# Performance work log

Hardware: AMD Instinct MI355X
Metric: run time of the kernel (lower is better)

The kernel has to match this reference:

```python
import jax, jax.numpy as jnp
import numpy as np

N = 10000      # nodes
E = 160000     # edges (avg degree 16)
D = 128        # channels
H = 4          # heads
C = 128        # per-head dim (PyG: out_channels per head = channels)
HC = H * C
EPS_SOFTMAX = 1e-16
EPS_NORM = 1e-5


def setup_inputs() -> dict:
    key = jax.random.key(0)
    ks = jax.random.split(key, 12)
    s = 1.0 / np.sqrt(D)
    sb = 1.0 / np.sqrt(3 * D)
    return {
        "x": jax.random.normal(ks[0], (N, D), jnp.float32),
        "edge_index": jax.random.randint(ks[1], (2, E), 0, N, dtype=jnp.int64),
        "Wq": jax.random.normal(ks[2], (D, HC), jnp.float32) * s,
        "bq": jnp.zeros((HC,), jnp.float32),
        "Wk": jax.random.normal(ks[3], (D, HC), jnp.float32) * s,
        "bk": jnp.zeros((HC,), jnp.float32),
        "Wv": jax.random.normal(ks[4], (D, HC), jnp.float32) * s,
        "bv": jnp.zeros((HC,), jnp.float32),
        "Wskip": jax.random.normal(ks[5], (D, D), jnp.float32) * s,
        "bskip": jnp.zeros((D,), jnp.float32),
        "Wbeta": jax.random.normal(ks[6], (3 * D,), jnp.float32) * sb,  # lin_beta, bias=False
        "gn_weight": jnp.ones((D,), jnp.float32),
        "gn_bias": jnp.zeros((D,), jnp.float32),
        "gn_mean_scale": jnp.ones((D,), jnp.float32),
    }


def reference(x, edge_index, Wq, bq, Wk, bk, Wv, bv, Wskip, bskip, Wbeta,
              gn_weight, gn_bias, gn_mean_scale):
    n = x.shape[0]
    src, dst = edge_index[0], edge_index[1]  # messages flow src(j) -> dst(i)

    # Projections [N,H,C]
    q = (x @ Wq + bq).reshape(n, H, C)
    k = (x @ Wk + bk).reshape(n, H, C)
    v = (x @ Wv + bv).reshape(n, H, C)

    # Per-edge attention logits [E,H]
    alpha = jnp.einsum('ehc,ehc->eh', q[dst], k[src]) / jnp.sqrt(jnp.float32(C))

    # Segment softmax over incoming edges of each dst node
    amax = jax.ops.segment_max(alpha, dst, num_segments=n)       # [N,H]
    amax = jnp.where(jnp.isfinite(amax), amax, 0.0)
    ex = jnp.exp(alpha - amax[dst])                              # [E,H]
    denom = jax.ops.segment_sum(ex, dst, num_segments=n)         # [N,H]
    attn = ex / (denom[dst] + EPS_SOFTMAX)                       # [E,H]

    # Weighted scatter-aggregate, then mean over heads (concat=False)
    msgs = attn[:, :, None] * v[src]                             # [E,H,C]
    out = jax.ops.segment_sum(msgs, dst, num_segments=n)         # [N,H,C]
    out = out.mean(axis=1)                                       # [N,D]

    # Beta-gated skip (PyG: beta = sigmoid(lin_beta([out, x_r, out - x_r])))
    skip = x @ Wskip + bskip
    beta = jax.nn.sigmoid(jnp.concatenate([out, skip, out - skip], axis=-1) @ Wbeta)
    beta = beta[:, None]
    out = beta * skip + (1.0 - beta) * out

    # GraphNorm (single graph): (x - mean_scale*mean) / sqrt(var + eps) * w + b
    mean = out.mean(axis=0)
    centered = out - gn_mean_scale * mean
    var = (centered * centered).mean(axis=0)
    out = gn_weight * centered / jnp.sqrt(var + EPS_NORM) + gn_bias

    # GELU (exact) + residual (shapes match); dropout is identity in eval
    out = jax.nn.gelu(out, approximate=False)
    return out + x
```

## Files before the change

### kernel.cpp

```cpp
#include <hip/hip_runtime.h>
#include <hip/hip_bf16.h>
#include <math.h>

#define D_DIM 128
#define HC_DIM 512
#define CAP 128
#define REP 4

typedef __attribute__((ext_vector_type(8))) short bf16x8;
typedef __attribute__((ext_vector_type(4))) float f32x4;
typedef __attribute__((ext_vector_type(2))) float f32x2;
typedef __attribute__((ext_vector_type(2))) _Float16 h16x2;

static __device__ __forceinline__ unsigned short f2bf(float f) {
  unsigned u = __float_as_uint(f);
  unsigned r = (u + 0x7fffu + ((u >> 16) & 1u)) >> 16;
  return (unsigned short)r;
}
static __device__ __forceinline__ float bflo(unsigned u) {
  return __uint_as_float(u << 16);
}
static __device__ __forceinline__ float bfhi(unsigned u) {
  return __uint_as_float(u & 0xffff0000u);
}

__global__ void prep_kernel(const float* __restrict__ x,
                            const float* __restrict__ Wq, const float* __restrict__ Wk,
                            const float* __restrict__ Wv, const float* __restrict__ Wskip,
                            const float* __restrict__ bq, const float* __restrict__ bk,
                            const float* __restrict__ bv, const float* __restrict__ bskip,
                            unsigned short* __restrict__ xb,
                            unsigned short* __restrict__ wcat,
                            float* __restrict__ bcat,
                            int* __restrict__ zbase, int zwords, int N) {
  int t = blockIdx.x * 256 + threadIdx.x;
  int X4 = N * 32;
  if (t < X4) {
    float4 f = *(const float4*)&x[t * 4];
    ushort4 o;
    o.x = f2bf(f.x); o.y = f2bf(f.y); o.z = f2bf(f.z); o.w = f2bf(f.w);
    *(ushort4*)&xb[t * 4] = o;
  } else if (t < X4 + 1664 * 128) {
    int widx = t - X4;
    if (widx < 3 * 65536) {
      int segi = widx >> 16;
      int r = widx & 65535;
      int kk = r >> 9;
      int m = r & 511;
      const float* W = (segi == 0) ? Wq : (segi == 1) ? Wk : Wv;
      wcat[(size_t)(segi * 512 + m) * 128 + kk] = f2bf(W[kk * 512 + m]);
    } else {
      int r = widx - 3 * 65536;
      int kk = r >> 7;
      int m = r & 127;
      wcat[(size_t)(1536 + m) * 128 + kk] = f2bf(Wskip[kk * 128 + m]);
    }
  } else if (t < X4 + 1664 * 128 + 1664) {
    int b = t - X4 - 1664 * 128;
    bcat[b] = (b < 512) ? bq[b] : (b < 1024) ? bk[b - 512]
            : (b < 1536) ? bv[b - 1024] : bskip[b - 1536];
  } else if (t < X4 + 1664 * 128 + 1664 + zwords) {
    zbase[t - X4 - 1664 * 128 - 1664] = 0;
  }
}

__global__ __launch_bounds__(256) void gemm_mfma_kernel(
    const unsigned short* __restrict__ Xb, const unsigned short* __restrict__ Wt,
    const float* __restrict__ bcat, unsigned short* __restrict__ qb,
    unsigned short* __restrict__ kf, unsigned char* __restrict__ v8,
    float* __restrict__ skip,
    const int* __restrict__ src, const int* __restrict__ dst,
    int* __restrict__ cnt, int* __restrict__ bsrc, int N, int E) {
  const int tid = threadIdx.x;
  {
    int nblk = gridDim.x * gridDim.y;
    int lb = blockIdx.y * gridDim.x + blockIdx.x;
    int per = (E + nblk - 1) / nblk;
    int e0 = lb * per;
    int e1 = min(e0 + per, E);
    for (int e = e0 + tid; e < e1; e += 256) {
      int d = dst[e];
      int p = atomicAdd(&cnt[d], 1);
      if (p < CAP) bsrc[d * CAP + p] = src[e];
    }
  }
  const int wave = tid >> 6, lane = tid & 63;
  const int l16 = lane & 15, quad = lane >> 4;
  const int row0 = (blockIdx.x * 4 + wave) * 64;
  const int col0 = blockIdx.y * 64;

  const unsigned short* xrow[4];
#pragma unroll
  for (int i = 0; i < 4; ++i) {
    int r = row0 + i * 16 + l16;
    if (r >= N) r = N - 1;
    xrow[i] = Xb + (size_t)r * 128;
  }
  const unsigned short* wrow[4];
  float bias[4];
#pragma unroll
  for (int j = 0; j < 4; ++j) {
    int c = col0 + j * 16 + l16;
    wrow[j] = Wt + (size_t)c * 128;
    bias[j] = bcat[c];
  }

  f32x4 acc[4][4] = {};
#pragma unroll
  for (int kk = 0; kk < 4; ++kk) {
    int k0 = kk * 32 + quad * 8;
    bf16x8 a[4], b[4];
#pragma unroll
    for (int i = 0; i < 4; ++i) a[i] = *(const bf16x8*)(xrow[i] + k0);
#pragma unroll
    for (int j = 0; j < 4; ++j) b[j] = *(const bf16x8*)(wrow[j] + k0);
#pragma unroll
    for (int i = 0; i < 4; ++i)
#pragma unroll
      for (int j = 0; j < 4; ++j)
        acc[i][j] = __builtin_amdgcn_mfma_f32_16x16x32_bf16(a[i], b[j], acc[i][j], 0, 0, 0);
  }

  const int kind = (col0 < 512) ? 0 : (col0 < 1024) ? 1 : (col0 < 1536) ? 2 : 3;
#pragma unroll
  for (int i = 0; i < 4; ++i) {
#pragma unroll
    for (int reg = 0; reg < 4; ++reg) {
      int r = row0 + i * 16 + quad * 4 + reg;
      if (r < N) {
#pragma unroll
        for (int j = 0; j < 4; ++j) {
          int cidx = col0 + j * 16 + l16;
          float val = acc[i][j][reg] + bias[j];
          if (kind == 0) {
            qb[(size_t)r * 512 + cidx] = f2bf(val);
          } else if (kind == 1) {
            _Float16 hv = (_Float16)val;
            kf[(size_t)r * 512 + cidx - 512] = *(unsigned short*)&hv;
          } else if (kind == 2) {
            int pk = __builtin_amdgcn_cvt_pk_fp8_f32(val, val, 0, false);
            v8[(size_t)r * 512 + cidx - 1024] = (unsigned char)pk;
          } else {
            skip[(size_t)r * 128 + cidx - 1536] = val;
          }
        }
      }
    }
  }
}

__global__ __launch_bounds__(256) void attn_combine_kernel(
    const unsigned short* __restrict__ qb, const unsigned short* __restrict__ kf,
    const unsigned char* __restrict__ v8, const int* __restrict__ cnt,
    const int* __restrict__ bsrc, const float* __restrict__ skip,
    const float* __restrict__ Wbeta, float* __restrict__ out2,
    float* __restrict__ colsum, float* __restrict__ colsq, int N) {
  __shared__ int eL[4][CAP];
  __shared__ float redS[4][128];
  __shared__ float redQ[4][128];
  int tid = threadIdx.x;
  int w = tid >> 6, lane = tid & 63;
  int node = blockIdx.x * 4 + w;
  bool nv = node < N;
  int nc = nv ? node : (N - 1);
  int g = lane >> 4, j = lane & 15;

  int count = nv ? min(cnt[nc], CAP) : 0;
  const int* bp = bsrc + (size_t)nc * CAP;
  for (int i = lane; i < count; i += 64) eL[w][i] = bp[i];

  const float qscale = 0.08838834764831845f * 1.4426950408889634f;
  float am0 = 0.f, am1 = 0.f, am2 = 0.f, am3 = 0.f;
  float am4 = 0.f, am5 = 0.f, am6 = 0.f, am7 = 0.f;

#pragma unroll 1
  for (int h = 0; h < 4; ++h) {
    int4 qi = *(const int4*)(qb + (size_t)nc * 512 + h * 128 + j * 8);
    h16x2 qh0, qh1, qh2, qh3;
    qh0[0] = (_Float16)(bflo(qi.x) * qscale); qh0[1] = (_Float16)(bfhi(qi.x) * qscale);
    qh1[0] = (_Float16)(bflo(qi.y) * qscale); qh1[1] = (_Float16)(bfhi(qi.y) * qscale);
    qh2[0] = (_Float16)(bflo(qi.z) * qscale); qh2[1] = (_Float16)(bfhi(qi.z) * qscale);
    qh3[0] = (_Float16)(bflo(qi.w) * qscale); qh3[1] = (_Float16)(bfhi(qi.w) * qscale);

    const unsigned short* kb = kf + h * 128 + j * 8;
    const unsigned char* vb = v8 + h * 128 + j * 8;
    float lsum = 0.f;
    float o0 = 0.f, o1 = 0.f, o2 = 0.f, o3 = 0.f;
    float o4 = 0.f, o5 = 0.f, o6 = 0.f, o7 = 0.f;

    if (count > 0) {
      int e = eL[w][(g < count) ? g : 0];
      uint4 kw = *(const uint4*)(kb + (size_t)e * 512);
      uint2 vw = *(const uint2*)(vb + (size_t)e * 512);
      for (int idx = 0; idx < count; idx += 4) {
        int rem = count - idx;
        int nrem = rem - 4;
        int en = (nrem > 0) ? eL[w][idx + 4 + ((g < nrem) ? g : 0)] : e;
        uint4 kwn = *(const uint4*)(kb + (size_t)en * 512);
        uint2 vwn = *(const uint2*)(vb + (size_t)en * 512);
        float p = __builtin_amdgcn_fdot2(qh0, *(h16x2*)&kw.x, 0.f, false);
        p = __builtin_amdgcn_fdot2(qh1, *(h16x2*)&kw.y, p, false);
        p = __builtin_amdgcn_fdot2(qh2, *(h16x2*)&kw.z, p, false);
        p = __builtin_amdgcn_fdot2(qh3, *(h16x2*)&kw.w, p, false);
        p += __shfl_xor(p, 1);
        p += __shfl_xor(p, 2);
        p += __shfl_xor(p, 4);
        p += __shfl_xor(p, 8);
        float a = (g < rem) ? p : -1e30f;
        float wgt = exp2f(a);
        f32x2 v01 = __builtin_amdgcn_cvt_pk_f32_fp8(vw.x, false);
        f32x2 v23 = __builtin_amdgcn_cvt_pk_f32_fp8(vw.x, true);
        f32x2 v45 = __builtin_amdgcn_cvt_pk_f32_fp8(vw.y, false);
        f32x2 v67 = __builtin_amdgcn_cvt_pk_f32_fp8(vw.y, true);
        lsum += wgt;
        o0 += wgt * v01.x; o1 += wgt * v01.y;
        o2 += wgt * v23.x; o3 += wgt * v23.y;
        o4 += wgt * v45.x; o5 += wgt * v45.y;
        o6 += wgt * v67.x; o7 += wgt * v67.y;
        kw = kwn; vw = vwn; e = en;
      }
    }
    o0 += __shfl_xor(o0, 16); o0 += __shfl_xor(o0, 32);
    o1 += __shfl_xor(o1, 16); o1 += __shfl_xor(o1, 32);
    o2 += __shfl_xor(o2, 16); o2 += __shfl_xor(o2, 32);
    o3 += __shfl_xor(o3, 16); o3 += __shfl_xor(o3, 32);
    o4 += __shfl_xor(o4, 16); o4 += __shfl_xor(o4, 32);
    o5 += __shfl_xor(o5, 16); o5 += __shfl_xor(o5, 32);
    o6 += __shfl_xor(o6, 16); o6 += __shfl_xor(o6, 32);
    o7 += __shfl_xor(o7, 16); o7 += __shfl_xor(o7, 32);
    lsum += __shfl_xor(lsum, 16); lsum += __shfl_xor(lsum, 32);
    float inv = 0.25f / (lsum + 1e-16f);
    am0 += o0 * inv; am1 += o1 * inv; am2 += o2 * inv; am3 += o3 * inv;
    am4 += o4 * inv; am5 += o5 * inv; am6 += o6 * inv; am7 += o7 * inv;
  }

  float4 sl = *(const float4*)&skip[(size_t)nc * 128 + j * 8];
  float4 sh = *(const float4*)&skip[(size_t)nc * 128 + j * 8 + 4];
  float4 wal = *(const float4*)&Wbeta[j * 8];
  float4 wah = *(const float4*)&Wbeta[j * 8 + 4];
  float4 wbl = *(const float4*)&Wbeta[128 + j * 8];
  float4 wbh = *(const float4*)&Wbeta[128 + j * 8 + 4];
  float4 wcl = *(const float4*)&Wbeta[256 + j * 8];
  float4 wch = *(const float4*)&Wbeta[256 + j * 8 + 4];
  float p = am0 * wal.x + sl.x * wbl.x + (am0 - sl.x) * wcl.x
          + am1 * wal.y + sl.y * wbl.y + (am1 - sl.y) * wcl.y
          + am2 * wal.z + sl.z * wbl.z + (am2 - sl.z) * wcl.z
          + am3 * wal.w + sl.w * wbl.w + (am3 - sl.w) * wcl.w
          + am4 * wah.x + sh.x * wbh.x + (am4 - sh.x) * wch.x
          + am5 * wah.y + sh.y * wbh.y + (am5 - sh.y) * wch.y
          + am6 * wah.z + sh.z * wbh.z + (am6 - sh.z) * wch.z
          + am7 * wah.w + sh.w * wbh.w + (am7 - sh.w) * wch.w;
  p += __shfl_xor(p, 1); p += __shfl_xor(p, 2);
  p += __shfl_xor(p, 4); p += __shfl_xor(p, 8);
  float beta = 1.f / (1.f + __expf(-p));
  float ob = 1.f - beta;
  float vm = nv ? 1.f : 0.f;
  float oc0 = (beta * sl.x + ob * am0) * vm;
  float oc1 = (beta * sl.y + ob * am1) * vm;
  float oc2 = (beta * sl.z + ob * am2) * vm;
  float oc3 = (beta * sl.w + ob * am3) * vm;
  float oc4 = (beta * sh.x + ob * am4) * vm;
  float oc5 = (beta * sh.y + ob * am5) * vm;
  float oc6 = (beta * sh.z + ob * am6) * vm;
  float oc7 = (beta * sh.w + ob * am7) * vm;

  if (g == 0) {
    float4 lo; lo.x = oc0; lo.y = oc1; lo.z = oc2; lo.w = oc3;
    float4 hi; hi.x = oc4; hi.y = oc5; hi.z = oc6; hi.w = oc7;
    if (nv) {
      *(float4*)&out2[(size_t)node * 128 + j * 8] = lo;
      *(float4*)&out2[(size_t)node * 128 + j * 8 + 4] = hi;
    }
    *(float4*)&redS[w][j * 8] = lo;
    *(float4*)&redS[w][j * 8 + 4] = hi;
    float4 ql; ql.x = oc0 * oc0; ql.y = oc1 * oc1; ql.z = oc2 * oc2; ql.w = oc3 * oc3;
    float4 qh; qh.x = oc4 * oc4; qh.y = oc5 * oc5; qh.z = oc6 * oc6; qh.w = oc7 * oc7;
    *(float4*)&redQ[w][j * 8] = ql;
    *(float4*)&redQ[w][j * 8 + 4] = qh;
  }
  __syncthreads();
  if (w == 0) {
    int c = lane * 2;
    float s0 = redS[0][c] + redS[1][c] + redS[2][c] + redS[3][c];
    float s1 = redS[0][c + 1] + redS[1][c + 1] + redS[2][c + 1] + redS[3][c + 1];
    float q0 = redQ[0][c] + redQ[1][c] + redQ[2][c] + redQ[3][c];
    float q1 = redQ[0][c + 1] + redQ[1][c + 1] + redQ[2][c + 1] + redQ[3][c + 1];
    int slot = (blockIdx.x & (REP - 1)) * 128;
    atomicAdd(&colsum[slot + c], s0);
    atomicAdd(&colsum[slot + c + 1], s1);
    atomicAdd(&colsq[slot + c], q0);
    atomicAdd(&colsq[slot + c + 1], q1);
  }
}

__global__ void final_kernel(const float* __restrict__ out2,
                             const float* __restrict__ colsum,
                             const float* __restrict__ colsq,
                             const float* __restrict__ gnw,
                             const float* __restrict__ gnb,
                             const float* __restrict__ gnms,
                             const float* __restrict__ x,
                             float* __restrict__ y, int total2, float invN) {
  int i = blockIdx.x * 256 + threadIdx.x;
  if (i < total2) {
    int c = (i & 63) * 2;
    float2 cs; cs.x = 0.f; cs.y = 0.f;
    float2 cq; cq.x = 0.f; cq.y = 0.f;
#pragma unroll
    for (int s = 0; s < REP; ++s) {
      float2 t = *(const float2*)&colsum[s * 128 + c];
      float2 u = *(const float2*)&colsq[s * 128 + c];
      cs.x += t.x; cs.y += t.y;
      cq.x += u.x; cq.y += u.y;
    }
    float2 gw = *(const float2*)&gnw[c];
    float2 gb = *(const float2*)&gnb[c];
    float2 gs = *(const float2*)&gnms[c];
    float mean0 = cs.x * invN, mean1 = cs.y * invN;
    float var0 = cq.x * invN - mean0 * mean0 * gs.x * (2.f - gs.x);
    float var1 = cq.y * invN - mean1 * mean1 * gs.y * (2.f - gs.y);
    float mul0 = gw.x / sqrtf(var0 + 1e-5f);
    float mul1 = gw.y / sqrtf(var1 + 1e-5f);
    float2 o = *(const float2*)&out2[i * 2];
    float2 xx = *(const float2*)&x[i * 2];
    float t0 = (o.x - gs.x * mean0) * mul0 + gb.x;
    float t1 = (o.y - gs.y * mean1) * mul1 + gb.y;
    float g0 = 0.5f * t0 * (1.f + erff(t0 * 0.70710678118654752f));
    float g1 = 0.5f * t1 * (1.f + erff(t1 * 0.70710678118654752f));
    float2 r; r.x = g0 + xx.x; r.y = g1 + xx.y;
    *(float2*)&y[i * 2] = r;
  }
}

extern "C" void kernel_launch(void* const* d_in, const int* in_sizes, int n_in,
                              void* d_out, int out_size, void* d_ws, size_t ws_size,
                              hipStream_t stream) {
  const float* x     = (const float*)d_in[0];
  const int*   ei    = (const int*)d_in[1];
  const float* Wq    = (const float*)d_in[2];
  const float* bq    = (const float*)d_in[3];
  const float* Wk    = (const float*)d_in[4];
  const float* bk    = (const float*)d_in[5];
  const float* Wv    = (const float*)d_in[6];
  const float* bv    = (const float*)d_in[7];
  const float* Wskip = (const float*)d_in[8];
  const float* bskip = (const float*)d_in[9];
  const float* Wbeta = (const float*)d_in[10];
  const float* gnw   = (const float*)d_in[11];
  const float* gnb   = (const float*)d_in[12];
  const float* gnms  = (const float*)d_in[13];

  const int N = in_sizes[0] / D_DIM;
  const int E = in_sizes[1] / 2;
  const int* src = ei;
  const int* dst = ei + E;

  char* p = (char*)d_ws;
  unsigned short* qb = (unsigned short*)p; p += (size_t)N * 512 * 2;
  unsigned short* kf = (unsigned short*)p; p += (size_t)N * 512 * 2;
  unsigned char*  v8 = (unsigned char*)p;  p += (size_t)N * 512;
  float*          skip = (float*)p;        p += (size_t)N * 128 * 4;
  float*          out2 = (float*)p;        p += (size_t)N * 128 * 4;
  int*   cnt    = (int*)p;   p += (size_t)N * 4;
  float* colsum = (float*)p; p += REP * 128 * 4;
  float* colsq  = (float*)p; p += REP * 128 * 4;
  int zwords = N + 2 * REP * 128;
  int* bsrc   = (int*)p;   p += (size_t)N * CAP * 4;
  unsigned short* wcat = (unsigned short*)p; p += (size_t)1664 * 128 * 2;
  float* bcat = (float*)p; p += 1664 * 4;
  unsigned short* xb = (unsigned short*)out2;

  int prepTotal = N * 32 + 1664 * 128 + 1664 + zwords;
  prep_kernel<<<(prepTotal + 255) / 256, 256, 0, stream>>>(
      x, Wq, Wk, Wv, Wskip, bq, bk, bv, bskip, xb, wcat, bcat, cnt, zwords, N);

  gemm_mfma_kernel<<<dim3(40, 26), 256, 0, stream>>>(
      xb, wcat, bcat, qb, kf, v8, skip, src, dst, cnt, bsrc, N, E);

  attn_combine_kernel<<<(N + 3) / 4, 256, 0, stream>>>(
      qb, kf, v8, cnt, bsrc, skip, Wbeta, out2, colsum, colsq, N);

  int total2 = N * D_DIM / 2;
  final_kernel<<<(total2 + 255) / 256, 256, 0, stream>>>(
      out2, colsum, colsq, gnw, gnb, gnms, x, (float*)d_out, total2, 1.f / (float)N);
}
```

Baseline: 183.6 us.

## Process all four heads in one edge loop instead of per-head passes

```diff
diff --git a/kernel.cpp b/kernel.cpp
--- a/kernel.cpp
+++ b/kernel.cpp
@@ -170,68 +170,93 @@
   for (int i = lane; i < count; i += 64) eL[w][i] = bp[i];
 
   const float qscale = 0.08838834764831845f * 1.4426950408889634f;
-  float am0 = 0.f, am1 = 0.f, am2 = 0.f, am3 = 0.f;
-  float am4 = 0.f, am5 = 0.f, am6 = 0.f, am7 = 0.f;
-
-#pragma unroll 1
+  h16x2 qh[4][4];
+#pragma unroll
   for (int h = 0; h < 4; ++h) {
     int4 qi = *(const int4*)(qb + (size_t)nc * 512 + h * 128 + j * 8);
-    h16x2 qh0, qh1, qh2, qh3;
-    qh0[0] = (_Float16)(bflo(qi.x) * qscale); qh0[1] = (_Float16)(bfhi(qi.x) * qscale);
-    qh1[0] = (_Float16)(bflo(qi.y) * qscale); qh1[1] = (_Float16)(bfhi(qi.y) * qscale);
-    qh2[0] = (_Float16)(bflo(qi.z) * qscale); qh2[1] = (_Float16)(bfhi(qi.z) * qscale);
-    qh3[0] = (_Float16)(bflo(qi.w) * qscale); qh3[1] = (_Float16)(bfhi(qi.w) * qscale);
-
-    const unsigned short* kb = kf + h * 128 + j * 8;
-    const unsigned char* vb = v8 + h * 128 + j * 8;
-    float lsum = 0.f;
-    float o0 = 0.f, o1 = 0.f, o2 = 0.f, o3 = 0.f;
-    float o4 = 0.f, o5 = 0.f, o6 = 0.f, o7 = 0.f;
-
-    if (count > 0) {
-      int e = eL[w][(g < count) ? g : 0];
-      uint4 kw = *(const uint4*)(kb + (size_t)e * 512);
-      uint2 vw = *(const uint2*)(vb + (size_t)e * 512);
-      for (int idx = 0; idx < count; idx += 4) {
-        int rem = count - idx;
-        int nrem = rem - 4;
-        int en = (nrem > 0) ? eL[w][idx + 4 + ((g < nrem) ? g : 0)] : e;
-        uint4 kwn = *(const uint4*)(kb + (size_t)en * 512);
-        uint2 vwn = *(const uint2*)(vb + (size_t)en * 512);
-        float p = __builtin_amdgcn_fdot2(qh0, *(h16x2*)&kw.x, 0.f, false);
-        p = __builtin_amdgcn_fdot2(qh1, *(h16x2*)&kw.y, p, false);
-        p = __builtin_amdgcn_fdot2(qh2, *(h16x2*)&kw.z, p, false);
-        p = __builtin_amdgcn_fdot2(qh3, *(h16x2*)&kw.w, p, false);
+    qh[h][0][0] = (_Float16)(bflo(qi.x) * qscale); qh[h][0][1] = (_Float16)(bfhi(qi.x) * qscale);
+    qh[h][1][0] = (_Float16)(bflo(qi.y) * qscale); qh[h][1][1] = (_Float16)(bfhi(qi.y) * qscale);
+    qh[h][2][0] = (_Float16)(bflo(qi.z) * qscale); qh[h][2][1] = (_Float16)(bfhi(qi.z) * qscale);
+    qh[h][3][0] = (_Float16)(bflo(qi.w) * qscale); qh[h][3][1] = (_Float16)(bfhi(qi.w) * qscale);
+  }
+
+  float o[4][8];
+  float lsum[4];
+#pragma unroll
+  for (int h = 0; h < 4; ++h) {
+    lsum[h] = 0.f;
+#pragma unroll
+    for (int r = 0; r < 8; ++r) o[h][r] = 0.f;
+  }
+
+  if (count > 0) {
+    int e = eL[w][(g < count) ? g : 0];
+    uint4 kw[4]; uint2 vw[4];
+    {
+      const unsigned short* kbe = kf + (size_t)e * 512 + j * 8;
+      const unsigned char* vbe = v8 + (size_t)e * 512 + j * 8;
+#pragma unroll
+      for (int h = 0; h < 4; ++h) {
+        kw[h] = *(const uint4*)(kbe + h * 128);
+        vw[h] = *(const uint2*)(vbe + h * 128);
+      }
+    }
+    for (int idx = 0; idx < count; idx += 4) {
+      int rem = count - idx;
+      int nrem = rem - 4;
+      int en = (nrem > 0) ? eL[w][idx + 4 + ((g < nrem) ? g : 0)] : e;
+      uint4 kwn[4]; uint2 vwn[4];
+      {
+        const unsigned short* kbe = kf + (size_t)en * 512 + j * 8;
+        const unsigned char* vbe = v8 + (size_t)en * 512 + j * 8;
+#pragma unroll
+        for (int h = 0; h < 4; ++h) {
+          kwn[h] = *(const uint4*)(kbe + h * 128);
+          vwn[h] = *(const uint2*)(vbe + h * 128);
+        }
+      }
+      bool act = (g < rem);
+#pragma unroll
+      for (int h = 0; h < 4; ++h) {
+        float p = __builtin_amdgcn_fdot2(qh[h][0], *(h16x2*)&kw[h].x, 0.f, false);
+        p = __builtin_amdgcn_fdot2(qh[h][1], *(h16x2*)&kw[h].y, p, false);
+        p = __builtin_amdgcn_fdot2(qh[h][2], *(h16x2*)&kw[h].z, p, false);
+        p = __builtin_amdgcn_fdot2(qh[h][3], *(h16x2*)&kw[h].w, p, false);
         p += __shfl_xor(p, 1);
         p += __shfl_xor(p, 2);
         p += __shfl_xor(p, 4);
         p += __shfl_xor(p, 8);
-        float a = (g < rem) ? p : -1e30f;
+        float a = act ? p : -1e30f;
         float wgt = exp2f(a);
-        f32x2 v01 = __builtin_amdgcn_cvt_pk_f32_fp8(vw.x, false);
-        f32x2 v23 = __builtin_amdgcn_cvt_pk_f32_fp8(vw.x, true);
-        f32x2 v45 = __builtin_amdgcn_cvt_pk_f32_fp8(vw.y, false);
-        f32x2 v67 = __builtin_amdgcn_cvt_pk_f32_fp8(vw.y, true);
-        lsum += wgt;
-        o0 += wgt * v01.x; o1 += wgt * v01.y;
-        o2 += wgt * v23.x; o3 += wgt * v23.y;
-        o4 += wgt * v45.x; o5 += wgt * v45.y;
-        o6 += wgt * v67.x; o7 += wgt * v67.y;
-        kw = kwn; vw = vwn; e = en;
+        f32x2 v01 = __builtin_amdgcn_cvt_pk_f32_fp8(vw[h].x, false);
+        f32x2 v23 = __builtin_amdgcn_cvt_pk_f32_fp8(vw[h].x, true);
+        f32x2 v45 = __builtin_amdgcn_cvt_pk_f32_fp8(vw[h].y, false);
+        f32x2 v67 = __builtin_amdgcn_cvt_pk_f32_fp8(vw[h].y, true);
+        lsum[h] += wgt;
+        o[h][0] += wgt * v01.x; o[h][1] += wgt * v01.y;
+        o[h][2] += wgt * v23.x; o[h][3] += wgt * v23.y;
+        o[h][4] += wgt * v45.x; o[h][5] += wgt * v45.y;
+        o[h][6] += wgt * v67.x; o[h][7] += wgt * v67.y;
+        kw[h] = kwn[h]; vw[h] = vwn[h];
       }
-    }
-    o0 += __shfl_xor(o0, 16); o0 += __shfl_xor(o0, 32);
-    o1 += __shfl_xor(o1, 16); o1 += __shfl_xor(o1, 32);
-    o2 += __shfl_xor(o2, 16); o2 += __shfl_xor(o2, 32);
-    o3 += __shfl_xor(o3, 16); o3 += __shfl_xor(o3, 32);
-    o4 += __shfl_xor(o4, 16); o4 += __shfl_xor(o4, 32);
-    o5 += __shfl_xor(o5, 16); o5 += __shfl_xor(o5, 32);
-    o6 += __shfl_xor(o6, 16); o6 += __shfl_xor(o6, 32);
-    o7 += __shfl_xor(o7, 16); o7 += __shfl_xor(o7, 32);
-    lsum += __shfl_xor(lsum, 16); lsum += __shfl_xor(lsum, 32);
-    float inv = 0.25f / (lsum + 1e-16f);
-    am0 += o0 * inv; am1 += o1 * inv; am2 += o2 * inv; am3 += o3 * inv;
-    am4 += o4 * inv; am5 += o5 * inv; am6 += o6 * inv; am7 += o7 * inv;
+      e = en;
+    }
+  }
+  float am[8];
+#pragma unroll
+  for (int r = 0; r < 8; ++r) am[r] = 0.f;
+#pragma unroll
+  for (int h = 0; h < 4; ++h) {
+#pragma unroll
+    for (int r = 0; r < 8; ++r) {
+      o[h][r] += __shfl_xor(o[h][r], 16);
+      o[h][r] += __shfl_xor(o[h][r], 32);
+    }
+    lsum[h] += __shfl_xor(lsum[h], 16);
+    lsum[h] += __shfl_xor(lsum[h], 32);
+    float inv = 0.25f / (lsum[h] + 1e-16f);
+#pragma unroll
+    for (int r = 0; r < 8; ++r) am[r] += o[h][r] * inv;
   }
 
   float4 sl = *(const float4*)&skip[(size_t)nc * 128 + j * 8];
@@ -242,27 +267,27 @@
   float4 wbh = *(const float4*)&Wbeta[128 + j * 8 + 4];
   float4 wcl = *(const float4*)&Wbeta[256 + j * 8];
   float4 wch = *(const float4*)&Wbeta[256 + j * 8 + 4];
-  float p = am0 * wal.x + sl.x * wbl.x + (am0 - sl.x) * wcl.x
-          + am1 * wal.y + sl.y * wbl.y + (am1 - sl.y) * wcl.y
-          + am2 * wal.z + sl.z * wbl.z + (am2 - sl.z) * wcl.z
-          + am3 * wal.w + sl.w * wbl.w + (am3 - sl.w) * wcl.w
-          + am4 * wah.x + sh.x * wbh.x + (am4 - sh.x) * wch.x
-          + am5 * wah.y + sh.y * wbh.y + (am5 - sh.y) * wch.y
-          + am6 * wah.z + sh.z * wbh.z + (am6 - sh.z) * wch.z
-          + am7 * wah.w + sh.w * wbh.w + (am7 - sh.w) * wch.w;
+  float p = am[0] * wal.x + sl.x * wbl.x + (am[0] - sl.x) * wcl.x
+          + am[1] * wal.y + sl.y * wbl.y + (am[1] - sl.y) * wcl.y
+          + am[2] * wal.z + sl.z * wbl.z + (am[2] - sl.z) * wcl.z
+          + am[3] * wal.w + sl.w * wbl.w + (am[3] - sl.w) * wcl.w
+          + am[4] * wah.x + sh.x * wbh.x + (am[4] - sh.x) * wch.x
+          + am[5] * wah.y + sh.y * wbh.y + (am[5] - sh.y) * wch.y
+          + am[6] * wah.z + sh.z * wbh.z + (am[6] - sh.z) * wch.z
+          + am[7] * wah.w + sh.w * wbh.w + (am[7] - sh.w) * wch.w;
   p += __shfl_xor(p, 1); p += __shfl_xor(p, 2);
   p += __shfl_xor(p, 4); p += __shfl_xor(p, 8);
   float beta = 1.f / (1.f + __expf(-p));
   float ob = 1.f - beta;
   float vm = nv ? 1.f : 0.f;
-  float oc0 = (beta * sl.x + ob * am0) * vm;
-  float oc1 = (beta * sl.y + ob * am1) * vm;
-  float oc2 = (beta * sl.z + ob * am2) * vm;
-  float oc3 = (beta * sl.w + ob * am3) * vm;
-  float oc4 = (beta * sh.x + ob * am4) * vm;
-  float oc5 = (beta * sh.y + ob * am5) * vm;
-  float oc6 = (beta * sh.z + ob * am6) * vm;
-  float oc7 = (beta * sh.w + ob * am7) * vm;
+  float oc0 = (beta * sl.x + ob * am[0]) * vm;
+  float oc1 = (beta * sl.y + ob * am[1]) * vm;
+  float oc2 = (beta * sl.z + ob * am[2]) * vm;
+  float oc3 = (beta * sl.w + ob * am[3]) * vm;
+  float oc4 = (beta * sh.x + ob * am[4]) * vm;
+  float oc5 = (beta * sh.y + ob * am[5]) * vm;
+  float oc6 = (beta * sh.z + ob * am[6]) * vm;
+  float oc7 = (beta * sh.w + ob * am[7]) * vm;
 
   if (g == 0) {
     float4 lo; lo.x = oc0; lo.y = oc1; lo.z = oc2; lo.w = oc3;
@@ -274,9 +299,9 @@
     *(float4*)&redS[w][j * 8] = lo;
     *(float4*)&redS[w][j * 8 + 4] = hi;
     float4 ql; ql.x = oc0 * oc0; ql.y = oc1 * oc1; ql.z = oc2 * oc2; ql.w = oc3 * oc3;
-    float4 qh; qh.x = oc4 * oc4; qh.y = oc5 * oc5; qh.z = oc6 * oc6; qh.w = oc7 * oc7;
+    float4 qh2; qh2.x = oc4 * oc4; qh2.y = oc5 * oc5; qh2.z = oc6 * oc6; qh2.w = oc7 * oc7;
     *(float4*)&redQ[w][j * 8] = ql;
-    *(float4*)&redQ[w][j * 8 + 4] = qh;
+    *(float4*)&redQ[w][j * 8 + 4] = qh2;
   }
   __syncthreads();
   if (w == 0) {
```

Result: faster. 179.1 us, median of 2 (-2.5%).

## Store K in fp8 and process all heads per lane in one pass

Applied to the files above, without the earlier changes.

```diff
diff --git a/kernel.cpp b/kernel.cpp
--- a/kernel.cpp
+++ b/kernel.cpp
@@ -10,7 +10,6 @@
 typedef __attribute__((ext_vector_type(8))) short bf16x8;
 typedef __attribute__((ext_vector_type(4))) float f32x4;
 typedef __attribute__((ext_vector_type(2))) float f32x2;
-typedef __attribute__((ext_vector_type(2))) _Float16 h16x2;
 
 static __device__ __forceinline__ unsigned short f2bf(float f) {
   unsigned u = __float_as_uint(f);
@@ -67,7 +66,7 @@
 __global__ __launch_bounds__(256) void gemm_mfma_kernel(
     const unsigned short* __restrict__ Xb, const unsigned short* __restrict__ Wt,
     const float* __restrict__ bcat, unsigned short* __restrict__ qb,
-    unsigned short* __restrict__ kf, unsigned char* __restrict__ v8,
+    unsigned char* __restrict__ k8, unsigned char* __restrict__ v8,
     float* __restrict__ skip,
     const int* __restrict__ src, const int* __restrict__ dst,
     int* __restrict__ cnt, int* __restrict__ bsrc, int N, int E) {
@@ -135,8 +134,8 @@
           if (kind == 0) {
             qb[(size_t)r * 512 + cidx] = f2bf(val);
           } else if (kind == 1) {
-            _Float16 hv = (_Float16)val;
-            kf[(size_t)r * 512 + cidx - 512] = *(unsigned short*)&hv;
+            int pk = __builtin_amdgcn_cvt_pk_fp8_f32(val, val, 0, false);
+            k8[(size_t)r * 512 + cidx - 512] = (unsigned char)pk;
           } else if (kind == 2) {
             int pk = __builtin_amdgcn_cvt_pk_fp8_f32(val, val, 0, false);
             v8[(size_t)r * 512 + cidx - 1024] = (unsigned char)pk;
@@ -149,8 +148,20 @@
   }
 }
 
+#define DOT8(u, r0, acc) { \
+  f32x2 l_ = __builtin_amdgcn_cvt_pk_f32_fp8((u), false); \
+  f32x2 h_ = __builtin_amdgcn_cvt_pk_f32_fp8((u), true); \
+  acc = fmaf(qf[r0], l_.x, acc); acc = fmaf(qf[(r0) + 1], l_.y, acc); \
+  acc = fmaf(qf[(r0) + 2], h_.x, acc); acc = fmaf(qf[(r0) + 3], h_.y, acc); }
+
+#define VACC(u, r0) { \
+  f32x2 l_ = __builtin_amdgcn_cvt_pk_f32_fp8((u), false); \
+  f32x2 h_ = __builtin_amdgcn_cvt_pk_f32_fp8((u), true); \
+  o[r0] = fmaf(wgt, l_.x, o[r0]); o[(r0) + 1] = fmaf(wgt, l_.y, o[(r0) + 1]); \
+  o[(r0) + 2] = fmaf(wgt, h_.x, o[(r0) + 2]); o[(r0) + 3] = fmaf(wgt, h_.y, o[(r0) + 3]); }
+
 __global__ __launch_bounds__(256) void attn_combine_kernel(
-    const unsigned short* __restrict__ qb, const unsigned short* __restrict__ kf,
+    const unsigned short* __restrict__ qb, const unsigned char* __restrict__ k8,
     const unsigned char* __restrict__ v8, const int* __restrict__ cnt,
     const int* __restrict__ bsrc, const float* __restrict__ skip,
     const float* __restrict__ Wbeta, float* __restrict__ out2,
@@ -170,113 +181,125 @@
   for (int i = lane; i < count; i += 64) eL[w][i] = bp[i];
 
   const float qscale = 0.08838834764831845f * 1.4426950408889634f;
-  float am0 = 0.f, am1 = 0.f, am2 = 0.f, am3 = 0.f;
-  float am4 = 0.f, am5 = 0.f, am6 = 0.f, am7 = 0.f;
-
-#pragma unroll 1
-  for (int h = 0; h < 4; ++h) {
-    int4 qi = *(const int4*)(qb + (size_t)nc * 512 + h * 128 + j * 8);
-    h16x2 qh0, qh1, qh2, qh3;
-    qh0[0] = (_Float16)(bflo(qi.x) * qscale); qh0[1] = (_Float16)(bfhi(qi.x) * qscale);
-    qh1[0] = (_Float16)(bflo(qi.y) * qscale); qh1[1] = (_Float16)(bfhi(qi.y) * qscale);
-    qh2[0] = (_Float16)(bflo(qi.z) * qscale); qh2[1] = (_Float16)(bfhi(qi.z) * qscale);
-    qh3[0] = (_Float16)(bflo(qi.w) * qscale); qh3[1] = (_Float16)(bfhi(qi.w) * qscale);
-
-    const unsigned short* kb = kf + h * 128 + j * 8;
-    const unsigned char* vb = v8 + h * 128 + j * 8;
-    float lsum = 0.f;
-    float o0 = 0.f, o1 = 0.f, o2 = 0.f, o3 = 0.f;
-    float o4 = 0.f, o5 = 0.f, o6 = 0.f, o7 = 0.f;
-
-    if (count > 0) {
-      int e = eL[w][(g < count) ? g : 0];
-      uint4 kw = *(const uint4*)(kb + (size_t)e * 512);
-      uint2 vw = *(const uint2*)(vb + (size_t)e * 512);
-      for (int idx = 0; idx < count; idx += 4) {
-        int rem = count - idx;
-        int nrem = rem - 4;
-        int en = (nrem > 0) ? eL[w][idx + 4 + ((g < nrem) ? g : 0)] : e;
-        uint4 kwn = *(const uint4*)(kb + (size_t)en * 512);
-        uint2 vwn = *(const uint2*)(vb + (size_t)en * 512);
-        float p = __builtin_amdgcn_fdot2(qh0, *(h16x2*)&kw.x, 0.f, false);
-        p = __builtin_amdgcn_fdot2(qh1, *(h16x2*)&kw.y, p, false);
-        p = __builtin_amdgcn_fdot2(qh2, *(h16x2*)&kw.z, p, false);
-        p = __builtin_amdgcn_fdot2(qh3, *(h16x2*)&kw.w, p, false);
-        p += __shfl_xor(p, 1);
-        p += __shfl_xor(p, 2);
-        p += __shfl_xor(p, 4);
-        p += __shfl_xor(p, 8);
-        float a = (g < rem) ? p : -1e30f;
-        float wgt = exp2f(a);
-        f32x2 v01 = __builtin_amdgcn_cvt_pk_f32_fp8(vw.x, false);
-        f32x2 v23 = __builtin_amdgcn_cvt_pk_f32_fp8(vw.x, true);
-        f32x2 v45 = __builtin_amdgcn_cvt_pk_f32_fp8(vw.y, false);
-        f32x2 v67 = __builtin_amdgcn_cvt_pk_f32_fp8(vw.y, true);
-        lsum += wgt;
-        o0 += wgt * v01.x; o1 += wgt * v01.y;
-        o2 += wgt * v23.x; o3 += wgt * v23.y;
-        o4 += wgt * v45.x; o5 += wgt * v45.y;
-        o6 += wgt * v67.x; o7 += wgt * v67.y;
-        kw = kwn; vw = vwn; e = en;
-      }
-    }
-    o0 += __shfl_xor(o0, 16); o0 += __shfl_xor(o0, 32);
-    o1 += __shfl_xor(o1, 16); o1 += __shfl_xor(o1, 32);
-    o2 += __shfl_xor(o2, 16); o2 += __shfl_xor(o2, 32);
-    o3 += __shfl_xor(o3, 16); o3 += __shfl_xor(o3, 32);
-    o4 += __shfl_xor(o4, 16); o4 += __shfl_xor(o4, 32);
-    o5 += __shfl_xor(o5, 16); o5 += __shfl_xor(o5, 32);
-    o6 += __shfl_xor(o6, 16); o6 += __shfl_xor(o6, 32);
-    o7 += __shfl_xor(o7, 16); o7 += __shfl_xor(o7, 32);
-    lsum += __shfl_xor(lsum, 16); lsum += __shfl_xor(lsum, 32);
-    float inv = 0.25f / (lsum + 1e-16f);
-    am0 += o0 * inv; am1 += o1 * inv; am2 += o2 * inv; am3 += o3 * inv;
-    am4 += o4 * inv; am5 += o5 * inv; am6 += o6 * inv; am7 += o7 * inv;
-  }
-
-  float4 sl = *(const float4*)&skip[(size_t)nc * 128 + j * 8];
-  float4 sh = *(const float4*)&skip[(size_t)nc * 128 + j * 8 + 4];
-  float4 wal = *(const float4*)&Wbeta[j * 8];
-  float4 wah = *(const float4*)&Wbeta[j * 8 + 4];
-  float4 wbl = *(const float4*)&Wbeta[128 + j * 8];
-  float4 wbh = *(const float4*)&Wbeta[128 + j * 8 + 4];
-  float4 wcl = *(const float4*)&Wbeta[256 + j * 8];
-  float4 wch = *(const float4*)&Wbeta[256 + j * 8 + 4];
-  float p = am0 * wal.x + sl.x * wbl.x + (am0 - sl.x) * wcl.x
-          + am1 * wal.y + sl.y * wbl.y + (am1 - sl.y) * wcl.y
-          + am2 * wal.z + sl.z * wbl.z + (am2 - sl.z) * wcl.z
-          + am3 * wal.w + sl.w * wbl.w + (am3 - sl.w) * wcl.w
-          + am4 * wah.x + sh.x * wbh.x + (am4 - sh.x) * wch.x
-          + am5 * wah.y + sh.y * wbh.y + (am5 - sh.y) * wch.y
-          + am6 * wah.z + sh.z * wbh.z + (am6 - sh.z) * wch.z
-          + am7 * wah.w + sh.w * wbh.w + (am7 - sh.w) * wch.w;
-  p += __shfl_xor(p, 1); p += __shfl_xor(p, 2);
-  p += __shfl_xor(p, 4); p += __shfl_xor(p, 8);
-  float beta = 1.f / (1.f + __expf(-p));
+  float qf[32];
+  {
+    const unsigned short* qrow = qb + (size_t)nc * 512 + (j >> 2) * 128 + (j & 3) * 32;
+    int4 q0 = *(const int4*)(qrow);
+    int4 q1 = *(const int4*)(qrow + 8);
+    int4 q2 = *(const int4*)(qrow + 16);
+    int4 q3 = *(const int4*)(qrow + 24);
+    qf[0] = bflo(q0.x) * qscale;  qf[1] = bfhi(q0.x) * qscale;
+    qf[2] = bflo(q0.y) * qscale;  qf[3] = bfhi(q0.y) * qscale;
+    qf[4] = bflo(q0.z) * qscale;  qf[5] = bfhi(q0.z) * qscale;
+    qf[6] = bflo(q0.w) * qscale;  qf[7] = bfhi(q0.w) * qscale;
+    qf[8] = bflo(q1.x) * qscale;  qf[9] = bfhi(q1.x) * qscale;
+    qf[10] = bflo(q1.y) * qscale; qf[11] = bfhi(q1.y) * qscale;
+    qf[12] = bflo(q1.z) * qscale; qf[13] = bfhi(q1.z) * qscale;
+    qf[14] = bflo(q1.w) * qscale; qf[15] = bfhi(q1.w) * qscale;
+    qf[16] = bflo(q2.x) * qscale; qf[17] = bfhi(q2.x) * qscale;
+    qf[18] = bflo(q2.y) * qscale; qf[19] = bfhi(q2.y) * qscale;
+    qf[20] = bflo(q2.z) * qscale; qf[21] = bfhi(q2.z) * qscale;
+    qf[22] = bflo(q2.w) * qscale; qf[23] = bfhi(q2.w) * qscale;
+    qf[24] = bflo(q3.x) * qscale; qf[25] = bfhi(q3.x) * qscale;
+    qf[26] = bflo(q3.y) * qscale; qf[27] = bfhi(q3.y) * qscale;
+    qf[28] = bflo(q3.z) * qscale; qf[29] = bfhi(q3.z) * qscale;
+    qf[30] = bflo(q3.w) * qscale; qf[31] = bfhi(q3.w) * qscale;
+  }
+
+  float o[32];
+#pragma unroll
+  for (int r = 0; r < 32; ++r) o[r] = 0.f;
+  float lsum = 0.f;
+
+  if (count > 0) {
+    int e = eL[w][(g < count) ? g : 0];
+    const unsigned char* kp = k8 + (size_t)e * 512 + j * 32;
+    const unsigned char* vp = v8 + (size_t)e * 512 + j * 32;
+    uint4 ka = *(const uint4*)kp;
+    uint4 kb = *(const uint4*)(kp + 16);
+    uint4 va = *(const uint4*)vp;
+    uint4 vb = *(const uint4*)(vp + 16);
+    for (int idx = 0; idx < count; idx += 4) {
+      int rem = count - idx;
+      int nrem = rem - 4;
+      int en = (nrem > 0) ? eL[w][idx + 4 + ((g < nrem) ? g : 0)] : e;
+      const unsigned char* kpn = k8 + (size_t)en * 512 + j * 32;
+      const unsigned char* vpn = v8 + (size_t)en * 512 + j * 32;
+      uint4 kan = *(const uint4*)kpn;
+      uint4 kbn = *(const uint4*)(kpn + 16);
+      uint4 van = *(const uint4*)vpn;
+      uint4 vbn = *(const uint4*)(vpn + 16);
+      float p0 = 0.f, p1 = 0.f, p2 = 0.f, p3 = 0.f;
+      DOT8(ka.x, 0, p0);  DOT8(ka.y, 4, p1);  DOT8(ka.z, 8, p2);  DOT8(ka.w, 12, p3);
+      DOT8(kb.x, 16, p0); DOT8(kb.y, 20, p1); DOT8(kb.z, 24, p2); DOT8(kb.w, 28, p3);
+      float p = (p0 + p1) + (p2 + p3);
+      p += __shfl_xor(p, 1);
+      p += __shfl_xor(p, 2);
+      float a = (g < rem) ? p : -1e30f;
+      float wgt = exp2f(a);
+      lsum += wgt;
+      VACC(va.x, 0);  VACC(va.y, 4);  VACC(va.z, 8);  VACC(va.w, 12);
+      VACC(vb.x, 16); VACC(vb.y, 20); VACC(vb.z, 24); VACC(vb.w, 28);
+      ka = kan; kb = kbn; va = van; vb = vbn; e = en;
+    }
+  }
+
+#pragma unroll
+  for (int r = 0; r < 32; ++r) {
+    o[r] += __shfl_xor(o[r], 16);
+    o[r] += __shfl_xor(o[r], 32);
+  }
+  lsum += __shfl_xor(lsum, 16);
+  lsum += __shfl_xor(lsum, 32);
+  float inv = 0.25f / (lsum + 1e-16f);
+#pragma unroll
+  for (int r = 0; r < 32; ++r) o[r] *= inv;
+#pragma unroll
+  for (int r = 0; r < 32; ++r) {
+    o[r] += __shfl_xor(o[r], 4);
+    o[r] += __shfl_xor(o[r], 8);
+  }
+
+  int d0 = (lane & 3) * 32;
+  const float* sp = skip + (size_t)nc * 128 + d0;
+  float s[32];
+  float pb = 0.f;
+#pragma unroll
+  for (int q4 = 0; q4 < 8; ++q4) {
+    float4 sv = *(const float4*)(sp + q4 * 4);
+    float4 wa = *(const float4*)(Wbeta + d0 + q4 * 4);
+    float4 wb = *(const float4*)(Wbeta + 128 + d0 + q4 * 4);
+    float4 wc = *(const float4*)(Wbeta + 256 + d0 + q4 * 4);
+    s[q4 * 4 + 0] = sv.x; s[q4 * 4 + 1] = sv.y;
+    s[q4 * 4 + 2] = sv.z; s[q4 * 4 + 3] = sv.w;
+    pb += o[q4 * 4 + 0] * wa.x + sv.x * wb.x + (o[q4 * 4 + 0] - sv.x) * wc.x
+        + o[q4 * 4 + 1] * wa.y + sv.y * wb.y + (o[q4 * 4 + 1] - sv.y) * wc.y
+        + o[q4 * 4 + 2] * wa.z + sv.z * wb.z + (o[q4 * 4 + 2] - sv.z) * wc.z
+        + o[q4 * 4 + 3] * wa.w + sv.w * wb.w + (o[q4 * 4 + 3] - sv.w) * wc.w;
+  }
+  pb += __shfl_xor(pb, 1);
+  pb += __shfl_xor(pb, 2);
+  float beta = 1.f / (1.f + __expf(-pb));
   float ob = 1.f - beta;
   float vm = nv ? 1.f : 0.f;
-  float oc0 = (beta * sl.x + ob * am0) * vm;
-  float oc1 = (beta * sl.y + ob * am1) * vm;
-  float oc2 = (beta * sl.z + ob * am2) * vm;
-  float oc3 = (beta * sl.w + ob * am3) * vm;
-  float oc4 = (beta * sh.x + ob * am4) * vm;
-  float oc5 = (beta * sh.y + ob * am5) * vm;
-  float oc6 = (beta * sh.z + ob * am6) * vm;
-  float oc7 = (beta * sh.w + ob * am7) * vm;
-
-  if (g == 0) {
-    float4 lo; lo.x = oc0; lo.y = oc1; lo.z = oc2; lo.w = oc3;
-    float4 hi; hi.x = oc4; hi.y = oc5; hi.z = oc6; hi.w = oc7;
-    if (nv) {
-      *(float4*)&out2[(size_t)node * 128 + j * 8] = lo;
-      *(float4*)&out2[(size_t)node * 128 + j * 8 + 4] = hi;
-    }
-    *(float4*)&redS[w][j * 8] = lo;
-    *(float4*)&redS[w][j * 8 + 4] = hi;
-    float4 ql; ql.x = oc0 * oc0; ql.y = oc1 * oc1; ql.z = oc2 * oc2; ql.w = oc3 * oc3;
-    float4 qh; qh.x = oc4 * oc4; qh.y = oc5 * oc5; qh.z = oc6 * oc6; qh.w = oc7 * oc7;
-    *(float4*)&redQ[w][j * 8] = ql;
-    *(float4*)&redQ[w][j * 8 + 4] = qh;
+  float oc[32];
+#pragma unroll
+  for (int r = 0; r < 32; ++r) oc[r] = (beta * s[r] + ob * o[r]) * vm;
+
+  if (lane < 4) {
+    size_t obase = (size_t)node * 128 + lane * 32;
+#pragma unroll
+    for (int q4 = 0; q4 < 8; ++q4) {
+      float4 vs;
+      vs.x = oc[q4 * 4 + 0]; vs.y = oc[q4 * 4 + 1];
+      vs.z = oc[q4 * 4 + 2]; vs.w = oc[q4 * 4 + 3];
+      if (nv) *(float4*)&out2[obase + q4 * 4] = vs;
+      *(float4*)&redS[w][lane * 32 + q4 * 4] = vs;
+      float4 vq;
+      vq.x = vs.x * vs.x; vq.y = vs.y * vs.y;
+      vq.z = vs.z * vs.z; vq.w = vs.w * vs.w;
+      *(float4*)&redQ[w][lane * 32 + q4 * 4] = vq;
+    }
   }
   __syncthreads();
   if (w == 0) {
@@ -357,7 +380,7 @@
 
   char* p = (char*)d_ws;
   unsigned short* qb = (unsigned short*)p; p += (size_t)N * 512 * 2;
-  unsigned short* kf = (unsigned short*)p; p += (size_t)N * 512 * 2;
+  unsigned char*  k8 = (unsigned char*)p;  p += (size_t)N * 512;
   unsigned char*  v8 = (unsigned char*)p;  p += (size_t)N * 512;
   float*          skip = (float*)p;        p += (size_t)N * 128 * 4;
   float*          out2 = (float*)p;        p += (size_t)N * 128 * 4;
@@ -375,10 +398,10 @@
       x, Wq, Wk, Wv, Wskip, bq, bk, bv, bskip, xb, wcat, bcat, cnt, zwords, N);
 
   gemm_mfma_kernel<<<dim3(40, 26), 256, 0, stream>>>(
-      xb, wcat, bcat, qb, kf, v8, skip, src, dst, cnt, bsrc, N, E);
+      xb, wcat, bcat, qb, k8, v8, skip, src, dst, cnt, bsrc, N, E);
 
   attn_combine_kernel<<<(N + 3) / 4, 256, 0, stream>>>(
-      qb, kf, v8, cnt, bsrc, skip, Wbeta, out2, colsum, colsq, N);
+      qb, k8, v8, cnt, bsrc, skip, Wbeta, out2, colsum, colsq, N);
 
   int total2 = N * D_DIM / 2;
   final_kernel<<<(total2 + 255) / 256, 256, 0, stream>>>(
```

After: 194.6 us. 6.0% more time.
